# Kernel tuning notes

Measured on AMD Instinct MI355X. Metric: run time of the kernel, lower is better.

Reference implementation:

```python
import jax, jax.numpy as jnp
import numpy as np

MIN_RES, MAX_RES, NUM_LOD, BAND_WIDTH = 16, 512, 8, 19
CODEBOOK_SIZE = 2 ** BAND_WIDTH  # 524288
_b = np.exp((np.log(MAX_RES) - np.log(MIN_RES)) / (NUM_LOD - 1))
LODS = [int(1 + np.floor(MIN_RES * _b ** l)) for l in range(NUM_LOD)]
SIZES = [min(CODEBOOK_SIZE, r ** 3) for r in LODS]
PRIMES = (1, 2654435761, 805459861)  # Instant-NGP spatial hash primes
N_PTS = 2_000_000

# corner offsets of the unit cube, [8,3]
_OFFS = np.array([[(i >> 2) & 1, (i >> 1) & 1, i & 1] for i in range(8)], dtype=np.int32)


def _hash_interp(p01, table, res, size):
    """Hashed trilinear interpolation for one LOD. p01:[N,3] in [0,1], table:[size]."""
    x = p01 * (res - 1)                                   # [N,3]
    c0 = jnp.clip(jnp.floor(x), 0, res - 2).astype(jnp.int32)
    frac = x - c0.astype(jnp.float32)                     # [N,3]
    offs = jnp.asarray(_OFFS)                             # [8,3]
    corners = (c0[:, None, :] + offs[None]).astype(jnp.uint32)  # [N,8,3]
    h = (corners[..., 0] * jnp.uint32(PRIMES[0])
         ^ corners[..., 1] * jnp.uint32(PRIMES[1])
         ^ corners[..., 2] * jnp.uint32(PRIMES[2]))
    idx = (h % jnp.uint32(size)).astype(jnp.int32)        # [N,8]
    feats = table[idx]                                    # [N,8] gather
    offf = offs.astype(jnp.float32)
    # trilinear weights: prod_d (frac if offset else 1-frac)
    w = jnp.prod(frac[:, None, :] * offf + (1.0 - frac[:, None, :]) * (1.0 - offf), axis=-1)
    return jnp.sum(w * feats, axis=-1)                    # [N]


def setup_inputs() -> dict:
    key = jax.random.key(0)
    k1, k2 = jax.random.split(key)
    pts = jax.random.uniform(k1, (N_PTS, 3), jnp.float32) * 2.0 - 1.0  # [-1,1]^3
    codebook = jax.random.normal(k2, (NUM_LOD, CODEBOOK_SIZE, 1), jnp.float32) * 0.01
    return {"pts": pts, "codebook": codebook}


def reference(pts, codebook):
    p01 = pts / 2.0 + 0.5                                  # normalize to [0,1]
    out = jnp.zeros(pts.shape[0], jnp.float32)
    for i, res in enumerate(LODS):                         # small static loop over LODs
        table = codebook[i, : SIZES[i], 0]                 # static slice -> actual table size
        out = out + _hash_interp(p01, table, res, SIZES[i])
    return out[:, None]                                    # [N, feat_dim=1]
```

## Files before the change

### kernel.cpp

```cpp
#include <hip/hip_runtime.h>
#include <math.h>


static constexpr unsigned CB_STRIDE = 524288u;
static constexpr int S0 = 4913;
static constexpr int S1 = 19683;
static constexpr unsigned WO2 = 0;
static constexpr unsigned WO3 = 85184;
static constexpr unsigned WO4 = 443104;
static constexpr unsigned WO5 = 967392;
static constexpr unsigned WO6 = 1491680;
static constexpr unsigned WO7 = 2015968;
static constexpr size_t WS_NEED_BYTES = 2540256u * 2u;

__device__ __forceinline__ unsigned short f32_to_bf16_rne(float f) {
    unsigned u = __float_as_uint(f);
    u = (u + 0x7FFFu + ((u >> 16) & 1u)) >> 16;
    return (unsigned short)u;
}
__device__ __forceinline__ float bf16_to_f32(unsigned short s) {
    return __uint_as_float(((unsigned)s) << 16);
}

struct I8 { unsigned a0, a1, a2, a3, a4, a5, a6, a7; };
struct R8 { unsigned short v0, v1, v2, v3, v4, v5, v6, v7; };
struct W3 { float x, y, z; };

template <unsigned SIZE>
__device__ __forceinline__ I8 idx8m(float p01x, float p01y, float p01z, int res, W3& fr)
{
    const float rm1 = (float)(res - 1);
    float xx = p01x * rm1, yy = p01y * rm1, zz = p01z * rm1;
    const float cmax = (float)(res - 2);
    float fx = fminf(fmaxf(floorf(xx), 0.0f), cmax);
    float fy = fminf(fmaxf(floorf(yy), 0.0f), cmax);
    float fz = fminf(fmaxf(floorf(zz), 0.0f), cmax);
    fr.x = xx - fx; fr.y = yy - fy; fr.z = zz - fz;
    const unsigned ix = (unsigned)(int)fx;
    const unsigned iy = (unsigned)(int)fy;
    const unsigned iz = (unsigned)(int)fz;
    const unsigned hy0 = iy * 2654435761u, hy1 = hy0 + 2654435761u;
    const unsigned hz0 = iz * 805459861u,  hz1 = hz0 + 805459861u;
    I8 o;
    o.a0 = (ix ^ hy0 ^ hz0) % SIZE;        o.a1 = (ix ^ hy0 ^ hz1) % SIZE;
    o.a2 = (ix ^ hy1 ^ hz0) % SIZE;        o.a3 = (ix ^ hy1 ^ hz1) % SIZE;
    o.a4 = ((ix+1u) ^ hy0 ^ hz0) % SIZE;   o.a5 = ((ix+1u) ^ hy0 ^ hz1) % SIZE;
    o.a6 = ((ix+1u) ^ hy1 ^ hz0) % SIZE;   o.a7 = ((ix+1u) ^ hy1 ^ hz1) % SIZE;
    return o;
}

__device__ __forceinline__ R8 gather8(const unsigned short* __restrict__ t, I8 o)
{
    R8 r;
    r.v0 = t[o.a0]; r.v1 = t[o.a1]; r.v2 = t[o.a2]; r.v3 = t[o.a3];
    r.v4 = t[o.a4]; r.v5 = t[o.a5]; r.v6 = t[o.a6]; r.v7 = t[o.a7];
    return r;
}

__device__ __forceinline__ float acc8(R8 r, W3 f)
{
    const float wx1 = f.x, wx0 = 1.0f - f.x;
    const float wy1 = f.y, wy0 = 1.0f - f.y;
    const float wz1 = f.z, wz0 = 1.0f - f.z;
    const float w00 = wy0 * wz0, w01 = wy0 * wz1;
    const float w10 = wy1 * wz0, w11 = wy1 * wz1;
    const float sx0 = bf16_to_f32(r.v0) * w00 + bf16_to_f32(r.v1) * w01
                    + bf16_to_f32(r.v2) * w10 + bf16_to_f32(r.v3) * w11;
    const float sx1 = bf16_to_f32(r.v4) * w00 + bf16_to_f32(r.v5) * w01
                    + bf16_to_f32(r.v6) * w10 + bf16_to_f32(r.v7) * w11;
    return wx0 * sx0 + wx1 * sx1;
}

template <int MODE>
__device__ __forceinline__ float lod_merged(float p01x, float p01y, float p01z,
                                            int res,
                                            const unsigned short* __restrict__ t)
{
    const float rm1 = (float)(res - 1);
    float xx = p01x * rm1, yy = p01y * rm1, zz = p01z * rm1;
    const float cmax = (float)(res - 2);
    float fx = fminf(fmaxf(floorf(xx), 0.0f), cmax);
    float fy = fminf(fmaxf(floorf(yy), 0.0f), cmax);
    float fz = fminf(fmaxf(floorf(zz), 0.0f), cmax);
    const float frx = xx - fx, fry = yy - fy, frz = zz - fz;
    const unsigned ix = (unsigned)(int)fx;
    const unsigned iy = (unsigned)(int)fy;
    const unsigned iz = (unsigned)(int)fz;

    const unsigned hy0 = iy * 2654435761u, hy1 = hy0 + 2654435761u;
    const unsigned hz0 = iz * 805459861u,  hz1 = hz0 + 805459861u;

    const unsigned h00 = ix ^ hy0 ^ hz0;
    const unsigned h01 = ix ^ hy0 ^ hz1;
    const unsigned h10 = ix ^ hy1 ^ hz0;
    const unsigned h11 = ix ^ hy1 ^ hz1;

    unsigned E00, E01, E10, E11;
    if (MODE == 0) {
        const unsigned bm = 524286u;
        E00 = h00 & bm; E01 = h01 & bm; E10 = h10 & bm; E11 = h11 & bm;
    } else {
        E00 = (h00 & ~1u) % 85184u; E01 = (h01 & ~1u) % 85184u;
        E10 = (h10 & ~1u) % 85184u; E11 = (h11 & ~1u) % 85184u;
    }

    const unsigned* t32 = reinterpret_cast<const unsigned*>(t);
    const unsigned p00 = t32[E00 >> 1];
    const unsigned p01 = t32[E01 >> 1];
    const unsigned p10 = t32[E10 >> 1];
    const unsigned p11 = t32[E11 >> 1];

    const bool oddx = (ix & 1u) != 0u;
    unsigned short q00 = 0, q01 = 0, q10 = 0, q11 = 0;
    if (oddx) {
        const unsigned g = ix + 1u;
        if (MODE == 0) {
            const unsigned m = 524287u;
            q00 = t[(g ^ hy0 ^ hz0) & m]; q01 = t[(g ^ hy0 ^ hz1) & m];
            q10 = t[(g ^ hy1 ^ hz0) & m]; q11 = t[(g ^ hy1 ^ hz1) & m];
        } else {
            q00 = t[(g ^ hy0 ^ hz0) % 85184u]; q01 = t[(g ^ hy0 ^ hz1) % 85184u];
            q10 = t[(g ^ hy1 ^ hz0) % 85184u]; q11 = t[(g ^ hy1 ^ hz1) % 85184u];
        }
    }

    const unsigned s00 = h00 & 1u, s01 = h01 & 1u, s10 = h10 & 1u, s11 = h11 & 1u;
    const float a00 = bf16_to_f32((unsigned short)(s00 ? (p00 >> 16) : (p00 & 0xffffu)));
    const float a01 = bf16_to_f32((unsigned short)(s01 ? (p01 >> 16) : (p01 & 0xffffu)));
    const float a10 = bf16_to_f32((unsigned short)(s10 ? (p10 >> 16) : (p10 & 0xffffu)));
    const float a11 = bf16_to_f32((unsigned short)(s11 ? (p11 >> 16) : (p11 & 0xffffu)));
    const float b00 = bf16_to_f32(oddx ? q00 : (unsigned short)(s00 ? (p00 & 0xffffu) : (p00 >> 16)));
    const float b01 = bf16_to_f32(oddx ? q01 : (unsigned short)(s01 ? (p01 & 0xffffu) : (p01 >> 16)));
    const float b10 = bf16_to_f32(oddx ? q10 : (unsigned short)(s10 ? (p10 & 0xffffu) : (p10 >> 16)));
    const float b11 = bf16_to_f32(oddx ? q11 : (unsigned short)(s11 ? (p11 & 0xffffu) : (p11 >> 16)));

    const float wx1 = frx, wx0 = 1.0f - frx;
    const float wy1 = fry, wy0 = 1.0f - fry;
    const float wz1 = frz, wz0 = 1.0f - frz;
    const float w00 = wy0 * wz0, w01 = wy0 * wz1;
    const float w10 = wy1 * wz0, w11 = wy1 * wz1;
    const float sx0 = a00 * w00 + a01 * w01 + a10 * w10 + a11 * w11;
    const float sx1 = b00 * w00 + b01 * w01 + b10 * w10 + b11 * w11;
    return wx0 * sx0 + wx1 * sx1;
}

__global__ __launch_bounds__(1024)
void HashGrid_convert_kernel(const float* __restrict__ codebook,
                             unsigned short* __restrict__ ws)
{
    const int lod = blockIdx.y;
    const int sizes[6] = {85184, 357911, 524288, 524288, 524288, 524288};
    const unsigned offs[6] = {WO2, WO3, WO4, WO5, WO6, WO7};
    const int idx = blockIdx.x * 1024 + threadIdx.x;
    if (idx < sizes[lod])
        ws[offs[lod] + idx] = f32_to_bf16_rne(codebook[(unsigned)(lod + 2) * CB_STRIDE + idx]);
}

__global__ __launch_bounds__(1024, 4)
void HashGrid_88278757802387_kernel(const float* __restrict__ pts,
                                    const float* __restrict__ codebook,
                                    const unsigned short* __restrict__ ws,
                                    float* __restrict__ out,
                                    int n, int res7)
{
    __shared__ unsigned short sm[S0 + S1];
    for (int j = threadIdx.x; j < S0 + S1; j += 1024)
        sm[j] = f32_to_bf16_rne(j < S0 ? codebook[j] : codebook[CB_STRIDE + (j - S0)]);
    __syncthreads();

    const int i = blockIdx.x * 1024 + threadIdx.x;
    if (i >= n) return;

    const float p01x = pts[3 * i + 0] * 0.5f + 0.5f;
    const float p01y = pts[3 * i + 1] * 0.5f + 0.5f;
    const float p01z = pts[3 * i + 2] * 0.5f + 0.5f;

    W3 fB, fL0, fL1;
    I8 oB = idx8m<357911u>(p01x, p01y, p01z, 71, fB);
    R8 rB = gather8(ws + WO3, oB);

    float acc = lod_merged<1>(p01x, p01y, p01z, 44,   ws + WO2);
    acc      += lod_merged<0>(p01x, p01y, p01z, 116,  ws + WO4);
    acc      += lod_merged<0>(p01x, p01y, p01z, 191,  ws + WO5);
    acc      += lod_merged<0>(p01x, p01y, p01z, 313,  ws + WO6);
    acc      += lod_merged<0>(p01x, p01y, p01z, res7, ws + WO7);

    I8 oL0 = idx8m<4913u >(p01x, p01y, p01z, 17, fL0);
    I8 oL1 = idx8m<19683u>(p01x, p01y, p01z, 27, fL1);
    R8 rL0 = gather8(sm, oL0);
    R8 rL1 = gather8(sm + S0, oL1);
    acc += acc8(rL0, fL0) + acc8(rL1, fL1);

    acc += acc8(rB, fB);

    out[i] = acc;
}

__global__ __launch_bounds__(1024, 4)
void HashGrid_fallback_kernel(const float* __restrict__ pts,
                              const float* __restrict__ codebook,
                              float* __restrict__ out,
                              int n, int res7)
{
    const int i = blockIdx.x * 1024 + threadIdx.x;
    if (i >= n) return;
    const float p01x = pts[3 * i + 0] * 0.5f + 0.5f;
    const float p01y = pts[3 * i + 1] * 0.5f + 0.5f;
    const float p01z = pts[3 * i + 2] * 0.5f + 0.5f;
    float acc = 0.0f;
    const int      reslist[8]  = {17, 27, 44, 71, 116, 191, 313, res7};
    const unsigned sizelist[8] = {4913u, 19683u, 85184u, 357911u, 524288u, 524288u, 524288u, 524288u};
    for (int l = 0; l < 8; ++l) {
        const int res = reslist[l];
        const unsigned size = sizelist[l];
        const float rm1 = (float)(res - 1);
        float xx = p01x * rm1, yy = p01y * rm1, zz = p01z * rm1;
        float fx = fminf(fmaxf(floorf(xx), 0.0f), (float)(res - 2));
        float fy = fminf(fmaxf(floorf(yy), 0.0f), (float)(res - 2));
        float fz = fminf(fmaxf(floorf(zz), 0.0f), (float)(res - 2));
        const float frx = xx - fx, fry = yy - fy, frz = zz - fz;
        const unsigned ix = (unsigned)(int)fx, iy = (unsigned)(int)fy, iz = (unsigned)(int)fz;
        const unsigned hy0 = iy * 2654435761u, hy1 = hy0 + 2654435761u;
        const unsigned hz0 = iz * 805459861u,  hz1 = hz0 + 805459861u;
        const unsigned o0 = (ix ^ hy0 ^ hz0) % size,      o1 = (ix ^ hy0 ^ hz1) % size;
        const unsigned o2 = (ix ^ hy1 ^ hz0) % size,      o3 = (ix ^ hy1 ^ hz1) % size;
        const unsigned o4 = ((ix+1u) ^ hy0 ^ hz0) % size, o5 = ((ix+1u) ^ hy0 ^ hz1) % size;
        const unsigned o6 = ((ix+1u) ^ hy1 ^ hz0) % size, o7 = ((ix+1u) ^ hy1 ^ hz1) % size;
        const float* tab = codebook + (unsigned)l * CB_STRIDE;
        const float wx1 = frx, wx0 = 1.0f - frx;
        const float wy1 = fry, wy0 = 1.0f - fry;
        const float wz1 = frz, wz0 = 1.0f - frz;
        const float w00 = wy0*wz0, w01 = wy0*wz1, w10 = wy1*wz0, w11 = wy1*wz1;
        acc += wx0 * (tab[o0]*w00 + tab[o1]*w01 + tab[o2]*w10 + tab[o3]*w11)
             + wx1 * (tab[o4]*w00 + tab[o5]*w01 + tab[o6]*w10 + tab[o7]*w11);
    }
    out[i] = acc;
}

extern "C" void kernel_launch(void* const* d_in, const int* in_sizes, int n_in,
                              void* d_out, int out_size, void* d_ws, size_t ws_size,
                              hipStream_t stream)
{
    const float* pts      = (const float*)d_in[0];
    const float* codebook = (const float*)d_in[1];
    float* out            = (float*)d_out;
    const int n = in_sizes[0] / 3;

    const double b = exp((log(512.0) - log(16.0)) / 7.0);
    const int res7 = (int)(1.0 + floor(16.0 * pow(b, 7.0)));

    const bool use_ws = (d_ws != nullptr) && (ws_size >= WS_NEED_BYTES);
    const int blocks = (n + 1023) / 1024;

    if (use_ws) {
        unsigned short* ws = (unsigned short*)d_ws;
        hipLaunchKernelGGL(HashGrid_convert_kernel, dim3(512, 6), dim3(1024),
                           0, stream, codebook, ws);
        hipLaunchKernelGGL(HashGrid_88278757802387_kernel, dim3(blocks), dim3(1024),
                           0, stream, pts, codebook, ws, out, n, res7);
    } else {
        hipLaunchKernelGGL(HashGrid_fallback_kernel, dim3(blocks), dim3(1024),
                           0, stream, pts, codebook, out, n, res7);
    }
}
```

Before: 353.1 us.

## Spatially bucket-sort points before hash-grid gathers to improve cache locality

Adds a counting-sort pipeline (zero histogram, histogram over a 32^3 spatial grid, single-block scan, atomic scatter) that reorders points into spatial buckets, stored as float4 with their original index. The main kernel then processes sorted points so that nearby threads hit nearby hash-table entries, and writes results back through the stored index. All eight LOD tables are now converted to bf16 in the workspace, with no shared-memory staging. The intent is to cut random global/L2 traffic from the gathers, at the cost of extra passes, atomics and a scattered output write. The new path runs only when the workspace is large enough, otherwise it falls back to the previous kernels.

```diff
diff --git a/kernel.cpp b/kernel.cpp
--- a/kernel.cpp
+++ b/kernel.cpp
@@ -5,13 +5,22 @@
 static constexpr unsigned CB_STRIDE = 524288u;
 static constexpr int S0 = 4913;
 static constexpr int S1 = 19683;
-static constexpr unsigned WO2 = 0;
-static constexpr unsigned WO3 = 85184;
-static constexpr unsigned WO4 = 443104;
-static constexpr unsigned WO5 = 967392;
-static constexpr unsigned WO6 = 1491680;
-static constexpr unsigned WO7 = 2015968;
-static constexpr size_t WS_NEED_BYTES = 2540256u * 2u;
+static constexpr unsigned O0 = 0;
+static constexpr unsigned O1 = 4928;
+static constexpr unsigned O2 = 24640;
+static constexpr unsigned O3 = 109824;
+static constexpr unsigned O4 = 467744;
+static constexpr unsigned O5 = 992032;
+static constexpr unsigned O6 = 1516320;
+static constexpr unsigned O7 = 2040608;
+static constexpr unsigned TBL_BYTES = 5129792u;
+static constexpr unsigned NB = 32768u;
+static constexpr unsigned OFF_H = TBL_BYTES;
+static constexpr unsigned OFF_P = OFF_H + NB * 4u;
+static constexpr size_t WS_MID_BYTES  = TBL_BYTES;
+__host__ __device__ static inline size_t ws_full_bytes(int n) {
+    return (size_t)OFF_P + (size_t)n * 16u;
+}
 
 __device__ __forceinline__ unsigned short f32_to_bf16_rne(float f) {
     unsigned u = __float_as_uint(f);
@@ -144,24 +153,121 @@
     return wx0 * sx0 + wx1 * sx1;
 }
 
+__device__ __forceinline__ unsigned bucket_key(float p01x, float p01y, float p01z)
+{
+    int ix = (int)(p01x * 32.0f); ix = ix < 0 ? 0 : (ix > 31 ? 31 : ix);
+    int iy = (int)(p01y * 32.0f); iy = iy < 0 ? 0 : (iy > 31 ? 31 : iy);
+    int iz = (int)(p01z * 32.0f); iz = iz < 0 ? 0 : (iz > 31 ? 31 : iz);
+    return ((unsigned)ix << 10) | ((unsigned)iy << 5) | (unsigned)iz;
+}
+
 __global__ __launch_bounds__(1024)
 void HashGrid_convert_kernel(const float* __restrict__ codebook,
                              unsigned short* __restrict__ ws)
 {
     const int lod = blockIdx.y;
-    const int sizes[6] = {85184, 357911, 524288, 524288, 524288, 524288};
-    const unsigned offs[6] = {WO2, WO3, WO4, WO5, WO6, WO7};
+    const int sizes[8] = {4913, 19683, 85184, 357911, 524288, 524288, 524288, 524288};
+    const unsigned offs[8] = {O0, O1, O2, O3, O4, O5, O6, O7};
     const int idx = blockIdx.x * 1024 + threadIdx.x;
     if (idx < sizes[lod])
-        ws[offs[lod] + idx] = f32_to_bf16_rne(codebook[(unsigned)(lod + 2) * CB_STRIDE + idx]);
-}
-
-__global__ __launch_bounds__(1024, 4)
-void HashGrid_88278757802387_kernel(const float* __restrict__ pts,
-                                    const float* __restrict__ codebook,
+        ws[offs[lod] + idx] = f32_to_bf16_rne(codebook[(unsigned)lod * CB_STRIDE + idx]);
+}
+
+__global__ __launch_bounds__(1024)
+void HashGrid_zero_hist(unsigned* __restrict__ hist)
+{
+    const int i = blockIdx.x * 1024 + threadIdx.x;
+    if (i < (int)NB) hist[i] = 0u;
+}
+
+__global__ __launch_bounds__(256)
+void HashGrid_hist_kernel(const float* __restrict__ pts, unsigned* __restrict__ hist, int n)
+{
+    const int i = blockIdx.x * 256 + threadIdx.x;
+    if (i >= n) return;
+    const float p01x = pts[3 * i + 0] * 0.5f + 0.5f;
+    const float p01y = pts[3 * i + 1] * 0.5f + 0.5f;
+    const float p01z = pts[3 * i + 2] * 0.5f + 0.5f;
+    atomicAdd(&hist[bucket_key(p01x, p01y, p01z)], 1u);
+}
+
+__global__ __launch_bounds__(1024)
+void HashGrid_scan_kernel(unsigned* __restrict__ h)
+{
+    __shared__ unsigned ps[1024];
+    const int t = threadIdx.x;
+    unsigned sum = 0;
+    for (int k = 0; k < 32; ++k) sum += h[t * 32 + k];
+    ps[t] = sum;
+    __syncthreads();
+    for (int off = 1; off < 1024; off <<= 1) {
+        unsigned v = ps[t];
+        unsigned add = (t >= off) ? ps[t - off] : 0u;
+        __syncthreads();
+        ps[t] = v + add;
+        __syncthreads();
+    }
+    unsigned run = (t == 0) ? 0u : ps[t - 1];
+    for (int k = 0; k < 32; ++k) {
+        const unsigned c = h[t * 32 + k];
+        h[t * 32 + k] = run;
+        run += c;
+    }
+}
+
+__global__ __launch_bounds__(256)
+void HashGrid_scatter_kernel(const float* __restrict__ pts, unsigned* __restrict__ off,
+                             float4* __restrict__ sorted, int n)
+{
+    const int i = blockIdx.x * 256 + threadIdx.x;
+    if (i >= n) return;
+    const float x = pts[3 * i + 0], y = pts[3 * i + 1], z = pts[3 * i + 2];
+    const float p01x = x * 0.5f + 0.5f;
+    const float p01y = y * 0.5f + 0.5f;
+    const float p01z = z * 0.5f + 0.5f;
+    const unsigned pos = atomicAdd(&off[bucket_key(p01x, p01y, p01z)], 1u);
+    sorted[pos] = make_float4(x, y, z, __uint_as_float((unsigned)i));
+}
+
+__global__ __launch_bounds__(256, 8)
+void HashGrid_88278757802387_kernel(const float4* __restrict__ sorted,
                                     const unsigned short* __restrict__ ws,
                                     float* __restrict__ out,
                                     int n, int res7)
+{
+    const int i = blockIdx.x * 256 + threadIdx.x;
+    if (i >= n) return;
+    const float4 p = sorted[i];
+    const float p01x = p.x * 0.5f + 0.5f;
+    const float p01y = p.y * 0.5f + 0.5f;
+    const float p01z = p.z * 0.5f + 0.5f;
+    const unsigned oidx = __float_as_uint(p.w);
+
+    W3 f0, f1, f2, f3;
+    I8 g0 = idx8m<4913u  >(p01x, p01y, p01z, 17, f0);
+    I8 g1 = idx8m<19683u >(p01x, p01y, p01z, 27, f1);
+    I8 g2 = idx8m<85184u >(p01x, p01y, p01z, 44, f2);
+    I8 g3 = idx8m<357911u>(p01x, p01y, p01z, 71, f3);
+    R8 r0 = gather8(ws + O0, g0);
+    R8 r1 = gather8(ws + O1, g1);
+    R8 r2 = gather8(ws + O2, g2);
+    R8 r3 = gather8(ws + O3, g3);
+    float acc = acc8(r0, f0) + acc8(r1, f1) + acc8(r2, f2) + acc8(r3, f3);
+
+    acc += lod_merged<0>(p01x, p01y, p01z, 116,  ws + O4);
+    acc += lod_merged<0>(p01x, p01y, p01z, 191,  ws + O5);
+    acc += lod_merged<0>(p01x, p01y, p01z, 313,  ws + O6);
+    acc += lod_merged<0>(p01x, p01y, p01z, res7, ws + O7);
+
+    out[oidx] = acc;
+}
+
+__global__ __launch_bounds__(1024, 4)
+void HashGrid_direct_kernel(const float* __restrict__ pts,
+                            const float* __restrict__ codebook,
+                            const unsigned short* __restrict__ ws,
+                            float* __restrict__ out,
+                            int n, int res7)
 {
     __shared__ unsigned short sm[S0 + S1];
     for (int j = threadIdx.x; j < S0 + S1; j += 1024)
@@ -177,20 +283,19 @@
 
     W3 fB, fL0, fL1;
     I8 oB = idx8m<357911u>(p01x, p01y, p01z, 71, fB);
-    R8 rB = gather8(ws + WO3, oB);
-
-    float acc = lod_merged<1>(p01x, p01y, p01z, 44,   ws + WO2);
-    acc      += lod_merged<0>(p01x, p01y, p01z, 116,  ws + WO4);
-    acc      += lod_merged<0>(p01x, p01y, p01z, 191,  ws + WO5);
-    acc      += lod_merged<0>(p01x, p01y, p01z, 313,  ws + WO6);
-    acc      += lod_merged<0>(p01x, p01y, p01z, res7, ws + WO7);
+    R8 rB = gather8(ws + O3, oB);
+
+    float acc = lod_merged<1>(p01x, p01y, p01z, 44,   ws + O2);
+    acc      += lod_merged<0>(p01x, p01y, p01z, 116,  ws + O4);
+    acc      += lod_merged<0>(p01x, p01y, p01z, 191,  ws + O5);
+    acc      += lod_merged<0>(p01x, p01y, p01z, 313,  ws + O6);
+    acc      += lod_merged<0>(p01x, p01y, p01z, res7, ws + O7);
 
     I8 oL0 = idx8m<4913u >(p01x, p01y, p01z, 17, fL0);
     I8 oL1 = idx8m<19683u>(p01x, p01y, p01z, 27, fL1);
     R8 rL0 = gather8(sm, oL0);
     R8 rL1 = gather8(sm + S0, oL1);
     acc += acc8(rL0, fL0) + acc8(rL1, fL1);
-
     acc += acc8(rB, fB);
 
     out[i] = acc;
@@ -249,17 +354,33 @@
     const double b = exp((log(512.0) - log(16.0)) / 7.0);
     const int res7 = (int)(1.0 + floor(16.0 * pow(b, 7.0)));
 
-    const bool use_ws = (d_ws != nullptr) && (ws_size >= WS_NEED_BYTES);
-    const int blocks = (n + 1023) / 1024;
-
-    if (use_ws) {
+    const int blocks256  = (n + 255) / 256;
+    const int blocks1024 = (n + 1023) / 1024;
+
+    if (d_ws != nullptr && ws_size >= ws_full_bytes(n)) {
         unsigned short* ws = (unsigned short*)d_ws;
-        hipLaunchKernelGGL(HashGrid_convert_kernel, dim3(512, 6), dim3(1024),
+        unsigned* hist = (unsigned*)((char*)d_ws + OFF_H);
+        float4* sorted = (float4*)((char*)d_ws + OFF_P);
+        hipLaunchKernelGGL(HashGrid_convert_kernel, dim3(512, 8), dim3(1024),
                            0, stream, codebook, ws);
-        hipLaunchKernelGGL(HashGrid_88278757802387_kernel, dim3(blocks), dim3(1024),
+        hipLaunchKernelGGL(HashGrid_zero_hist, dim3(NB / 1024), dim3(1024),
+                           0, stream, hist);
+        hipLaunchKernelGGL(HashGrid_hist_kernel, dim3(blocks256), dim3(256),
+                           0, stream, pts, hist, n);
+        hipLaunchKernelGGL(HashGrid_scan_kernel, dim3(1), dim3(1024),
+                           0, stream, hist);
+        hipLaunchKernelGGL(HashGrid_scatter_kernel, dim3(blocks256), dim3(256),
+                           0, stream, pts, hist, sorted, n);
+        hipLaunchKernelGGL(HashGrid_88278757802387_kernel, dim3(blocks256), dim3(256),
+                           0, stream, sorted, ws, out, n, res7);
+    } else if (d_ws != nullptr && ws_size >= WS_MID_BYTES) {
+        unsigned short* ws = (unsigned short*)d_ws;
+        hipLaunchKernelGGL(HashGrid_convert_kernel, dim3(512, 8), dim3(1024),
+                           0, stream, codebook, ws);
+        hipLaunchKernelGGL(HashGrid_direct_kernel, dim3(blocks1024), dim3(1024),
                            0, stream, pts, codebook, ws, out, n, res7);
     } else {
-        hipLaunchKernelGGL(HashGrid_fallback_kernel, dim3(blocks), dim3(1024),
+        hipLaunchKernelGGL(HashGrid_fallback_kernel, dim3(blocks1024), dim3(1024),
                            0, stream, pts, codebook, out, n, res7);
     }
 }
```

Measured after the change: 577.2 us. +63.5%, slower.
